# Performance work log

Hardware: AMD Instinct MI355X
Metric: run time of the kernel (lower is better)

Reference implementation:

```python
import jax, jax.numpy as jnp
import numpy as np

L, N, E, H = 2048, 4, 256, 4
D = E // H  # head_dim


def setup_inputs() -> dict:
    key = jax.random.key(0)
    ks = jax.random.split(key, 8)
    s = 1.0 / np.sqrt(E)
    return {
        "x": jax.random.normal(ks[0], (L, N, E), jnp.float32),
        "pos_emb": jax.random.normal(ks[1], (1, 2 * L - 1, E), jnp.float32),
        "in_proj_w": jax.random.normal(ks[2], (3 * E, E), jnp.float32) * s,
        "in_proj_b": jnp.zeros((3 * E,), jnp.float32),
        "pos_w": jax.random.normal(ks[3], (E, E), jnp.float32) * s,
        "pos_bias_u": jax.random.normal(ks[4], (H, D), jnp.float32) * s,
        "pos_bias_v": jax.random.normal(ks[5], (H, D), jnp.float32) * s,
        "out_proj_w": jax.random.normal(ks[6], (E, E), jnp.float32) * s,
        "out_proj_b": jnp.zeros((E,), jnp.float32),
    }


def _rel_shift(bd):
    # bd: (N, H, L, 2L-1) -> (N, H, L, L); out[...,i,j] = bd[...,i, L-1-i+j]
    l = bd.shape[2]
    idx = (l - 1) - jnp.arange(l)[:, None] + jnp.arange(l)[None, :]  # (L, L)
    return jnp.take_along_axis(bd, idx[None, None, :, :], axis=-1)


def reference(x, pos_emb, in_proj_w, in_proj_b, pos_w, pos_bias_u,
              pos_bias_v, out_proj_w, out_proj_b):
    scaling = 1.0 / jnp.sqrt(jnp.asarray(D, x.dtype))
    qkv = x @ in_proj_w.T + in_proj_b                # (L, N, 3E)
    q, k, v = jnp.split(qkv, 3, axis=-1)
    q = q * scaling
    # (L,N,E) -> (N,H,L,D)
    q = q.reshape(L, N, H, D).transpose(1, 2, 0, 3)
    k = k.reshape(L, N, H, D).transpose(1, 2, 0, 3)
    v = v.reshape(L, N, H, D).transpose(1, 2, 0, 3)
    # positional projection: (1, 2L-1, E) -> (H, 2L-1, D)
    p = (pos_emb @ pos_w.T).reshape(2 * L - 1, H, D).transpose(1, 0, 2)
    q_u = q + pos_bias_u[None, :, None, :]
    q_v = q + pos_bias_v[None, :, None, :]
    matrix_ac = jnp.einsum('bhld,bhsd->bhls', q_u, k)          # (N,H,L,L)
    matrix_bd = jnp.einsum('bhld,hnd->bhln', q_v, p)           # (N,H,L,2L-1)
    matrix_bd = _rel_shift(matrix_bd)                          # (N,H,L,L)
    scores = matrix_ac + matrix_bd
    attn = jax.nn.softmax(scores, axis=-1)
    out = jnp.einsum('bhls,bhsd->bhld', attn, v)               # (N,H,L,D)
    out = out.transpose(2, 0, 1, 3).reshape(L, N, E)
    return out @ out_proj_w.T + out_proj_b
```

## Files before the change

### kernel.cpp

```cpp
#include <hip/hip_runtime.h>
#include <math.h>
#include <stdint.h>


typedef __attribute__((ext_vector_type(8))) _Float16 half8;
typedef __attribute__((ext_vector_type(4))) float f32x4;
typedef unsigned short u16;
typedef unsigned int u32;

namespace {
constexpr int L_SEQ  = 2048;
constexpr int NB     = 4;
constexpr int EMB    = 256;
constexpr int NH     = 4;
constexpr int HD     = 64;
constexpr int E3     = 768;
constexpr int M_ROWS = L_SEQ * NB;
constexpr int P_ROWS = 2 * L_SEQ - 1;
}

__device__ __forceinline__ u16 f2h(float x) {
    _Float16 h = (_Float16)x;
    return __builtin_bit_cast(u16, h);
}
__device__ __forceinline__ u32 pk2(float a, float b) {
    return (u32)f2h(a) | ((u32)f2h(b) << 16);
}

template <int MODE>
__global__ __launch_bounds__(256, 2) void proj_gemm(
        const void* __restrict__ Ap, const float* __restrict__ W,
        const float* __restrict__ Wb,
        const float* __restrict__ u_bias, const float* __restrict__ v_bias,
        u16* __restrict__ quB, u16* __restrict__ qvB,
        u16* __restrict__ kB,  u16* __restrict__ vtB,
        u16* __restrict__ o16, float* __restrict__ outf) {
    constexpr int NTILES = (MODE == 0) ? 12 : 4;
    __shared__ __align__(16) u16 ws[64 * 256];

    const int t    = threadIdx.x;
    const int lane = t & 63;
    const int w    = t >> 6;
    const int il   = lane & 15;
    const int g    = lane >> 4;

    const int qq = gridDim.x >> 3;
    const int logical = (blockIdx.x & 7) * qq + (blockIdx.x >> 3);
    const int mt = logical / NTILES, nt = logical % NTILES;
    const int m0 = mt * 64, n0 = nt * 64;

    {
        const int kc = (t & 31) * 8;
        const int rb = t >> 5;
        #pragma unroll
        for (int rr = 0; rr < 8; ++rr) {
            const int row = rb * 8 + rr;
            const float* wr = &W[(size_t)(n0 + row) * 256 + kc];
            float4 f0 = *(const float4*)&wr[0];
            float4 f1 = *(const float4*)&wr[4];
            uint4 pk = make_uint4(pk2(f0.x, f0.y), pk2(f0.z, f0.w),
                                  pk2(f1.x, f1.y), pk2(f1.z, f1.w));
            *(uint4*)((char*)ws + row * 512 + ((kc * 2) ^ ((row & 7) << 4))) = pk;
        }
    }

    const int m = m0 + w * 16 + il;
    half8 bfrag[8];
    if (MODE == 2) {
        const u16* arow = (const u16*)Ap + (size_t)m * 256;
        #pragma unroll
        for (int c = 0; c < 8; ++c)
            bfrag[c] = *(const half8*)&arow[c * 32 + g * 8];
    } else {
        const int mld = (MODE == 1 && m > P_ROWS - 1) ? (P_ROWS - 1) : m;
        const float* arow = (const float*)Ap + (size_t)mld * 256;
        #pragma unroll
        for (int c = 0; c < 8; ++c) {
            float4 f0 = *(const float4*)&arow[c * 32 + g * 8];
            float4 f1 = *(const float4*)&arow[c * 32 + g * 8 + 4];
            uint4 pk = make_uint4(pk2(f0.x, f0.y), pk2(f0.z, f0.w),
                                  pk2(f1.x, f1.y), pk2(f1.z, f1.w));
            bfrag[c] = __builtin_bit_cast(half8, pk);
        }
    }
    __syncthreads();

    f32x4 acc[4] = {};
    __builtin_amdgcn_s_setprio(1);
    #pragma unroll
    for (int c = 0; c < 8; ++c) {
        #pragma unroll
        for (int jt = 0; jt < 4; ++jt) {
            const int row = jt * 16 + il;
            half8 af = *(const half8*)((const char*)ws + row * 512 +
                                       ((c * 64 + g * 16) ^ ((row & 7) << 4)));
            acc[jt] = __builtin_amdgcn_mfma_f32_16x16x32_f16(af, bfrag[c], acc[jt], 0, 0, 0);
        }
    }
    __builtin_amdgcn_s_setprio(0);

    float av[4][4];
    #pragma unroll
    for (int jt = 0; jt < 4; ++jt)
        #pragma unroll
        for (int r = 0; r < 4; ++r)
            av[jt][r] = acc[jt][r] +
                ((MODE != 1) ? Wb[n0 + jt * 16 + g * 4 + r] : 0.f);

    if (MODE == 0) {
        const int seg = nt >> 2;
        const int h   = nt & 3;
        const int i = m >> 2, b = m & 3, bh = b * 4 + h;
        const size_t obase = (((size_t)bh << 11) + i) * 64;
        if (seg == 0) {
            #pragma unroll
            for (int jt = 0; jt < 4; ++jt) {
                const int d0 = jt * 16 + g * 4;
                float uu[4], vv[4];
                #pragma unroll
                for (int r = 0; r < 4; ++r) {
                    uu[r] = av[jt][r] * 0.125f + u_bias[h * 64 + d0 + r];
                    vv[r] = av[jt][r] * 0.125f + v_bias[h * 64 + d0 + r];
                }
                *(uint2*)&quB[obase + d0] = make_uint2(pk2(uu[0], uu[1]), pk2(uu[2], uu[3]));
                *(uint2*)&qvB[obase + d0] = make_uint2(pk2(vv[0], vv[1]), pk2(vv[2], vv[3]));
            }
        } else if (seg == 1) {
            #pragma unroll
            for (int jt = 0; jt < 4; ++jt) {
                const int d0 = jt * 16 + g * 4;
                *(uint2*)&kB[obase + d0] =
                    make_uint2(pk2(av[jt][0], av[jt][1]), pk2(av[jt][2], av[jt][3]));
            }
        } else {
            __syncthreads();
            u16* vt = ws;
            #pragma unroll
            for (int jt = 0; jt < 4; ++jt) {
                *(uint2*)&vt[(w * 16 + il) * 68 + jt * 16 + g * 4] =
                    make_uint2(pk2(av[jt][0], av[jt][1]), pk2(av[jt][2], av[jt][3]));
            }
            __syncthreads();
            const int d = t & 63, bsel = t >> 6;
            u32 pkx[8];
            #pragma unroll
            for (int p2 = 0; p2 < 8; ++p2)
                pkx[p2] = (u32)vt[(p2 * 8 + bsel) * 68 + d] |
                          ((u32)vt[(p2 * 8 + 4 + bsel) * 68 + d] << 16);
            u16* dst = &vtB[(((size_t)(bsel * 4 + h)) * 64 + d) * 2048 + (m0 >> 2)];
            *(uint4*)&dst[0] = make_uint4(pkx[0], pkx[1], pkx[2], pkx[3]);
            *(uint4*)&dst[8] = make_uint4(pkx[4], pkx[5], pkx[6], pkx[7]);
        }
    } else if (MODE == 1) {
        const int h = nt;
        if (m < P_ROWS) {
            #pragma unroll
            for (int jt = 0; jt < 4; ++jt) {
                const int d0 = jt * 16 + g * 4;
                *(uint2*)&o16[((size_t)h * P_ROWS + m) * 64 + d0] =
                    make_uint2(pk2(av[jt][0], av[jt][1]), pk2(av[jt][2], av[jt][3]));
            }
        }
    } else {
        float* orow = &outf[(size_t)m * 256 + n0];
        #pragma unroll
        for (int jt = 0; jt < 4; ++jt) {
            float4 o = make_float4(av[jt][0], av[jt][1], av[jt][2], av[jt][3]);
            *(float4*)&orow[jt * 16 + g * 4] = o;
        }
    }
}

__global__ __launch_bounds__(256, 2) void attn_mfma(
        const u16* __restrict__ quB, const u16* __restrict__ qvB,
        const u16* __restrict__ kB,  const u16* __restrict__ vtB,
        const u16* __restrict__ pB,  u16* __restrict__ attn_out) {
    __shared__ __align__(16) u16   k_s[64 * 64];
    __shared__ __align__(16) u16   v_s[64 * 64];
    __shared__ __align__(16) u16   p_s[128 * 64];
    __shared__ __align__(16) float bd_s[4][16 * 84];
    __shared__ __align__(16) u16   prob_s[4][16 * 64];

    const int t    = threadIdx.x;
    const int lane = t & 63;
    const int w    = t >> 6;
    const int il   = lane & 15;
    const int g    = lane >> 4;

    const int logical = ((blockIdx.x & 7) << 6) + (blockIdx.x >> 3);
    const int bh = logical >> 5;
    const int i0 = (logical & 31) * 64;
    const int b  = bh >> 2, h = bh & 3;

    half8 qu_f[2], qv_f[2];
    {
        const size_t qrow = ((size_t)bh * L_SEQ + i0 + w * 16 + il) * HD;
        qu_f[0] = *(const half8*)&quB[qrow + g * 8];
        qu_f[1] = *(const half8*)&quB[qrow + 32 + g * 8];
        qv_f[0] = *(const half8*)&qvB[qrow + g * 8];
        qv_f[1] = *(const half8*)&qvB[qrow + 32 + g * 8];
    }

    const int r0w = 48 - 16 * w;
    int krd[4][2], prd[5][2], pbrd[2], pwr[4];
    #pragma unroll
    for (int x4 = 0; x4 < 4; ++x4)
        #pragma unroll
        for (int c = 0; c < 2; ++c) {
            int row = x4 * 16 + il;
            krd[x4][c] = row * 128 + ((c * 64 + g * 16) ^ ((row & 7) << 4));
        }
    #pragma unroll
    for (int rt = 0; rt < 5; ++rt)
        #pragma unroll
        for (int c = 0; c < 2; ++c) {
            int row = r0w + rt * 16 + il;
            prd[rt][c] = row * 128 + ((c * 64 + g * 16) ^ ((row & 7) << 4));
        }
    #pragma unroll
    for (int c = 0; c < 2; ++c)
        pbrd[c] = il * 128 + ((c * 64 + g * 16) ^ ((il & 7) << 4));
    #pragma unroll
    for (int jt = 0; jt < 4; ++jt)
        pwr[jt] = il * 128 + (((jt * 16 + g * 4) * 2) ^ ((il & 7) << 4));
    const int bdwr = il * 84 + g * 4;
    const int bdrd = il * 83 + 15 + g * 4;

    f32x4 outacc[4] = {};
    float m_run = -INFINITY, l_run = 0.f;

    for (int kt = 0; kt < 32; ++kt) {
        const int j0 = kt * 64;
        const int nbase = 1984 - i0 + j0;
        __syncthreads();
        {
            const int rw = t >> 3;
            const int a  = t & 7;
            #pragma unroll
            for (int kr = 0; kr < 2; ++kr) {
                const int j = kr * 32 + rw;
                uint4 val = *(const uint4*)&kB[((size_t)bh * L_SEQ + j0 + j) * HD + a * 8];
                *(uint4*)((char*)k_s + (j * 128 + ((a * 16) ^ ((j & 7) << 4)))) = val;
            }
            #pragma unroll
            for (int vr = 0; vr < 2; ++vr) {
                const int d = vr * 32 + rw;
                uint4 val = *(const uint4*)&vtB[((size_t)bh * HD + d) * L_SEQ + j0 + a * 8];
                *(uint4*)((char*)v_s + (d * 128 + ((a * 16) ^ ((d & 7) << 4)))) = val;
            }
            #pragma unroll
            for (int pr = 0; pr < 4; ++pr) {
                const int r = pr * 32 + rw;
                int n = nbase + r; n = n > (P_ROWS - 1) ? (P_ROWS - 1) : n;
                uint4 val = *(const uint4*)&pB[((size_t)h * P_ROWS + n) * HD + a * 8];
                *(uint4*)((char*)p_s + (r * 128 + ((a * 16) ^ ((r & 7) << 4)))) = val;
            }
        }
        __syncthreads();

        __builtin_amdgcn_s_setprio(1);
        #pragma unroll
        for (int rt = 0; rt < 5; ++rt) {
            f32x4 acc = {};
            #pragma unroll
            for (int c = 0; c < 2; ++c) {
                half8 a = *(const half8*)((const char*)p_s + prd[rt][c]);
                acc = __builtin_amdgcn_mfma_f32_16x16x32_f16(a, qv_f[c], acc, 0, 0, 0);
            }
            *(f32x4*)&bd_s[w][bdwr + rt * 16] = acc;
        }
        __builtin_amdgcn_s_setprio(0);

        float sreg[16];
        __builtin_amdgcn_s_setprio(1);
        #pragma unroll
        for (int jt = 0; jt < 4; ++jt) {
            f32x4 acc = {};
            #pragma unroll
            for (int c = 0; c < 2; ++c) {
                half8 a = *(const half8*)((const char*)k_s + krd[jt][c]);
                acc = __builtin_amdgcn_mfma_f32_16x16x32_f16(a, qu_f[c], acc, 0, 0, 0);
            }
            #pragma unroll
            for (int tt = 0; tt < 4; ++tt)
                sreg[jt * 4 + tt] = acc[tt] + bd_s[w][bdrd + jt * 16 + tt];
        }
        __builtin_amdgcn_s_setprio(0);

        float mx = sreg[0];
        #pragma unroll
        for (int z = 1; z < 16; ++z) mx = fmaxf(mx, sreg[z]);
        mx = fmaxf(mx, __shfl_xor(mx, 16));
        mx = fmaxf(mx, __shfl_xor(mx, 32));
        const float m_new = fmaxf(m_run, mx);
        const float corr = __expf(m_run - m_new);
        float lsum = 0.f;
        #pragma unroll
        for (int z = 0; z < 16; ++z) { sreg[z] = __expf(sreg[z] - m_new); lsum += sreg[z]; }
        lsum += __shfl_xor(lsum, 16);
        lsum += __shfl_xor(lsum, 32);
        l_run = l_run * corr + lsum;
        m_run = m_new;
        #pragma unroll
        for (int dt = 0; dt < 4; ++dt) outacc[dt] *= corr;

        #pragma unroll
        for (int jt = 0; jt < 4; ++jt) {
            u32 lo = pk2(sreg[jt * 4 + 0], sreg[jt * 4 + 1]);
            u32 hi = pk2(sreg[jt * 4 + 2], sreg[jt * 4 + 3]);
            *(uint2*)((char*)&prob_s[w][0] + pwr[jt]) = make_uint2(lo, hi);
        }

        half8 pfrag[2];
        #pragma unroll
        for (int c = 0; c < 2; ++c)
            pfrag[c] = *(const half8*)((const char*)&prob_s[w][0] + pbrd[c]);
        __builtin_amdgcn_s_setprio(1);
        #pragma unroll
        for (int dt = 0; dt < 4; ++dt) {
            #pragma unroll
            for (int c = 0; c < 2; ++c) {
                half8 a = *(const half8*)((const char*)v_s + krd[dt][c]);
                outacc[dt] = __builtin_amdgcn_mfma_f32_16x16x32_f16(a, pfrag[c], outacc[dt], 0, 0, 0);
            }
        }
        __builtin_amdgcn_s_setprio(0);
    }

    const float inv = 1.f / l_run;
    const int m = (i0 + w * 16 + il) * NB + b;
    u16* orow = &attn_out[(size_t)m * EMB + h * HD];
    #pragma unroll
    for (int dt = 0; dt < 4; ++dt) {
        u32 lo = pk2(outacc[dt][0] * inv, outacc[dt][1] * inv);
        u32 hi = pk2(outacc[dt][2] * inv, outacc[dt][3] * inv);
        *(uint2*)&orow[dt * 16 + g * 4] = make_uint2(lo, hi);
    }
}

extern "C" void kernel_launch(void* const* d_in, const int* in_sizes, int n_in,
                              void* d_out, int out_size, void* d_ws, size_t ws_size,
                              hipStream_t stream) {
    const float* x        = (const float*)d_in[0];
    const float* pos_emb  = (const float*)d_in[1];
    const float* in_w     = (const float*)d_in[2];
    const float* in_b     = (const float*)d_in[3];
    const float* pos_w    = (const float*)d_in[4];
    const float* u_bias   = (const float*)d_in[5];
    const float* v_bias   = (const float*)d_in[6];
    const float* out_w    = (const float*)d_in[7];
    const float* out_b    = (const float*)d_in[8];
    float* out = (float*)d_out;

    u16* quB   = (u16*)d_ws;
    u16* qvB   = quB + (size_t)16 * L_SEQ * HD;
    u16* kB    = qvB + (size_t)16 * L_SEQ * HD;
    u16* vtB   = kB  + (size_t)16 * L_SEQ * HD;
    u16* pB    = vtB + (size_t)16 * L_SEQ * HD;
    u16* attnb = pB  + (size_t)NH * P_ROWS * HD;

    proj_gemm<0><<<dim3(128 * 12), 256, 0, stream>>>(
        x, in_w, in_b, u_bias, v_bias, quB, qvB, kB, vtB, nullptr, nullptr);
    proj_gemm<1><<<dim3(64 * 4), 256, 0, stream>>>(
        pos_emb, pos_w, nullptr, nullptr, nullptr,
        nullptr, nullptr, nullptr, nullptr, pB, nullptr);
    attn_mfma<<<dim3(512), 256, 0, stream>>>(quB, qvB, kB, vtB, pB, attnb);
    proj_gemm<2><<<dim3(128 * 4), 256, 0, stream>>>(
        attnb, out_w, out_b, nullptr, nullptr,
        nullptr, nullptr, nullptr, nullptr, nullptr, out);
}
```

Measured before the change: 169.9 us.

## Reuse weight tiles across M subtiles, stage coalesced stores, prefetch attention tiles

The projection GEMM now processes several 64-row M subtiles per block (MSUB), so each block loads and converts the weight tile once. The next A subtile is prefetched into registers while the current one computes. Q/K/V outputs are staged through a shared scratch buffer so global writes become full 16-byte coalesced rows. The V transpose now covers a full 64-position span. The attention kernel prefetches the next K/V/P tile into registers during the current tile's compute. This trades fewer blocks and more register and LDS use, which may lower occupancy, for reduced redundant weight loading and better overlap of global loads.

```diff
diff --git a/kernel.cpp b/kernel.cpp
--- a/kernel.cpp
+++ b/kernel.cpp
@@ -27,7 +27,7 @@
     return (u32)f2h(a) | ((u32)f2h(b) << 16);
 }
 
-template <int MODE>
+template <int MODE, int MSUB>
 __global__ __launch_bounds__(256, 2) void proj_gemm(
         const void* __restrict__ Ap, const float* __restrict__ W,
         const float* __restrict__ Wb,
@@ -35,8 +35,10 @@
         u16* __restrict__ quB, u16* __restrict__ qvB,
         u16* __restrict__ kB,  u16* __restrict__ vtB,
         u16* __restrict__ o16, float* __restrict__ outf) {
-    constexpr int NTILES = (MODE == 0) ? 12 : 4;
+    constexpr int NT   = (MODE == 0) ? 12 : 4;
+    constexpr int SCRN = (MODE == 0) ? (4 * 64 * 72) : (MODE == 1 ? 64 * 72 : 8);
     __shared__ __align__(16) u16 ws[64 * 256];
+    __shared__ __align__(16) u16 scr[SCRN];
 
     const int t    = threadIdx.x;
     const int lane = t & 63;
@@ -46,15 +48,49 @@
 
     const int qq = gridDim.x >> 3;
     const int logical = (blockIdx.x & 7) * qq + (blockIdx.x >> 3);
-    const int mt = logical / NTILES, nt = logical % NTILES;
-    const int m0 = mt * 64, n0 = nt * 64;
-
+    const int mg = logical / NT, nt = logical % NT;
+    const int n0 = nt * 64;
+
+    half8 bf[2][8];
+    float4 ra[2][8], rb[2][8];
+
+    auto issueA = [&](int s, int p) {
+        const int m_ = (mg * MSUB + s) * 64 + w * 16 + il;
+        if constexpr (MODE == 2) {
+            const u16* ar = (const u16*)Ap + (size_t)m_ * 256;
+            #pragma unroll
+            for (int c = 0; c < 8; ++c)
+                bf[p][c] = *(const half8*)&ar[c * 32 + g * 8];
+        } else {
+            const int mld = (MODE == 1 && m_ > P_ROWS - 1) ? (P_ROWS - 1) : m_;
+            const float* ar = (const float*)Ap + (size_t)mld * 256;
+            #pragma unroll
+            for (int c = 0; c < 8; ++c) {
+                ra[p][c] = *(const float4*)&ar[c * 32 + g * 8];
+                rb[p][c] = *(const float4*)&ar[c * 32 + g * 8 + 4];
+            }
+        }
+    };
+    auto packA = [&](int p) {
+        if constexpr (MODE != 2) {
+            #pragma unroll
+            for (int c = 0; c < 8; ++c) {
+                uint4 pk = make_uint4(pk2(ra[p][c].x, ra[p][c].y),
+                                      pk2(ra[p][c].z, ra[p][c].w),
+                                      pk2(rb[p][c].x, rb[p][c].y),
+                                      pk2(rb[p][c].z, rb[p][c].w));
+                bf[p][c] = __builtin_bit_cast(half8, pk);
+            }
+        }
+    };
+
+    issueA(0, 0);
     {
         const int kc = (t & 31) * 8;
-        const int rb = t >> 5;
+        const int rb_ = t >> 5;
         #pragma unroll
         for (int rr = 0; rr < 8; ++rr) {
-            const int row = rb * 8 + rr;
+            const int row = rb_ * 8 + rr;
             const float* wr = &W[(size_t)(n0 + row) * 256 + kc];
             float4 f0 = *(const float4*)&wr[0];
             float4 f1 = *(const float4*)&wr[4];
@@ -63,110 +99,152 @@
             *(uint4*)((char*)ws + row * 512 + ((kc * 2) ^ ((row & 7) << 4))) = pk;
         }
     }
-
-    const int m = m0 + w * 16 + il;
-    half8 bfrag[8];
-    if (MODE == 2) {
-        const u16* arow = (const u16*)Ap + (size_t)m * 256;
-        #pragma unroll
-        for (int c = 0; c < 8; ++c)
-            bfrag[c] = *(const half8*)&arow[c * 32 + g * 8];
-    } else {
-        const int mld = (MODE == 1 && m > P_ROWS - 1) ? (P_ROWS - 1) : m;
-        const float* arow = (const float*)Ap + (size_t)mld * 256;
+    packA(0);
+    __syncthreads();
+
+    const int seg = (MODE == 0) ? (nt >> 2) : 0;
+    const int h   = (MODE == 0) ? (nt & 3) : nt;
+
+    #pragma unroll
+    for (int s = 0; s < MSUB; ++s) {
+        if (s + 1 < MSUB) issueA(s + 1, (s + 1) & 1);
+
+        f32x4 acc[4] = {};
         #pragma unroll
         for (int c = 0; c < 8; ++c) {
-            float4 f0 = *(const float4*)&arow[c * 32 + g * 8];
-            float4 f1 = *(const float4*)&arow[c * 32 + g * 8 + 4];
-            uint4 pk = make_uint4(pk2(f0.x, f0.y), pk2(f0.z, f0.w),
-                                  pk2(f1.x, f1.y), pk2(f1.z, f1.w));
-            bfrag[c] = __builtin_bit_cast(half8, pk);
-        }
-    }
-    __syncthreads();
-
-    f32x4 acc[4] = {};
-    __builtin_amdgcn_s_setprio(1);
-    #pragma unroll
-    for (int c = 0; c < 8; ++c) {
-        #pragma unroll
-        for (int jt = 0; jt < 4; ++jt) {
-            const int row = jt * 16 + il;
-            half8 af = *(const half8*)((const char*)ws + row * 512 +
-                                       ((c * 64 + g * 16) ^ ((row & 7) << 4)));
-            acc[jt] = __builtin_amdgcn_mfma_f32_16x16x32_f16(af, bfrag[c], acc[jt], 0, 0, 0);
-        }
-    }
-    __builtin_amdgcn_s_setprio(0);
-
-    float av[4][4];
-    #pragma unroll
-    for (int jt = 0; jt < 4; ++jt)
-        #pragma unroll
-        for (int r = 0; r < 4; ++r)
-            av[jt][r] = acc[jt][r] +
-                ((MODE != 1) ? Wb[n0 + jt * 16 + g * 4 + r] : 0.f);
-
-    if (MODE == 0) {
-        const int seg = nt >> 2;
-        const int h   = nt & 3;
-        const int i = m >> 2, b = m & 3, bh = b * 4 + h;
-        const size_t obase = (((size_t)bh << 11) + i) * 64;
-        if (seg == 0) {
+            #pragma unroll
+            for (int jt = 0; jt < 4; ++jt) {
+                const int row = jt * 16 + il;
+                half8 af = *(const half8*)((const char*)ws + row * 512 +
+                                           ((c * 64 + g * 16) ^ ((row & 7) << 4)));
+                acc[jt] = __builtin_amdgcn_mfma_f32_16x16x32_f16(af, bf[s & 1][c], acc[jt], 0, 0, 0);
+            }
+        }
+
+        float av[4][4];
+        #pragma unroll
+        for (int jt = 0; jt < 4; ++jt)
+            #pragma unroll
+            for (int r = 0; r < 4; ++r)
+                av[jt][r] = acc[jt][r] +
+                    ((MODE != 1) ? Wb[n0 + jt * 16 + g * 4 + r] : 0.f);
+
+        const int s64  = (mg * MSUB + s) * 64;
+        const int mloc = w * 16 + il;
+
+        if constexpr (MODE == 0) {
+            if (seg == 0) {
+                const int i0g = s64 >> 2;
+                __syncthreads();
+                #pragma unroll
+                for (int jt = 0; jt < 4; ++jt) {
+                    const int d0 = jt * 16 + g * 4;
+                    float uu[4];
+                    #pragma unroll
+                    for (int r = 0; r < 4; ++r)
+                        uu[r] = av[jt][r] * 0.125f + u_bias[h * 64 + d0 + r];
+                    *(uint2*)&scr[mloc * 72 + d0] = make_uint2(pk2(uu[0], uu[1]), pk2(uu[2], uu[3]));
+                }
+                __syncthreads();
+                {
+                    const int b_ = t >> 6, iL = (t >> 2) & 15, dq = (t & 3) * 16;
+                    uint4 v0 = *(const uint4*)&scr[(iL * 4 + b_) * 72 + dq];
+                    uint4 v1 = *(const uint4*)&scr[(iL * 4 + b_) * 72 + dq + 8];
+                    u16* dst = &quB[(((size_t)(b_ * 4 + h)) * 2048 + i0g + iL) * 64 + dq];
+                    *(uint4*)&dst[0] = v0; *(uint4*)&dst[8] = v1;
+                }
+                __syncthreads();
+                #pragma unroll
+                for (int jt = 0; jt < 4; ++jt) {
+                    const int d0 = jt * 16 + g * 4;
+                    float vv[4];
+                    #pragma unroll
+                    for (int r = 0; r < 4; ++r)
+                        vv[r] = av[jt][r] * 0.125f + v_bias[h * 64 + d0 + r];
+                    *(uint2*)&scr[mloc * 72 + d0] = make_uint2(pk2(vv[0], vv[1]), pk2(vv[2], vv[3]));
+                }
+                __syncthreads();
+                {
+                    const int b_ = t >> 6, iL = (t >> 2) & 15, dq = (t & 3) * 16;
+                    uint4 v0 = *(const uint4*)&scr[(iL * 4 + b_) * 72 + dq];
+                    uint4 v1 = *(const uint4*)&scr[(iL * 4 + b_) * 72 + dq + 8];
+                    u16* dst = &qvB[(((size_t)(b_ * 4 + h)) * 2048 + i0g + iL) * 64 + dq];
+                    *(uint4*)&dst[0] = v0; *(uint4*)&dst[8] = v1;
+                }
+            } else if (seg == 1) {
+                const int i0g = s64 >> 2;
+                __syncthreads();
+                #pragma unroll
+                for (int jt = 0; jt < 4; ++jt) {
+                    const int d0 = jt * 16 + g * 4;
+                    *(uint2*)&scr[mloc * 72 + d0] =
+                        make_uint2(pk2(av[jt][0], av[jt][1]), pk2(av[jt][2], av[jt][3]));
+                }
+                __syncthreads();
+                {
+                    const int b_ = t >> 6, iL = (t >> 2) & 15, dq = (t & 3) * 16;
+                    uint4 v0 = *(const uint4*)&scr[(iL * 4 + b_) * 72 + dq];
+                    uint4 v1 = *(const uint4*)&scr[(iL * 4 + b_) * 72 + dq + 8];
+                    u16* dst = &kB[(((size_t)(b_ * 4 + h)) * 2048 + i0g + iL) * 64 + dq];
+                    *(uint4*)&dst[0] = v0; *(uint4*)&dst[8] = v1;
+                }
+            } else {
+                const int b_ = il & 3;
+                const int jl = s * 16 + w * 4 + (il >> 2);
+                #pragma unroll
+                for (int jt = 0; jt < 4; ++jt) {
+                    const int d0 = jt * 16 + g * 4;
+                    *(uint2*)&scr[(b_ * 64 + jl) * 72 + d0] =
+                        make_uint2(pk2(av[jt][0], av[jt][1]), pk2(av[jt][2], av[jt][3]));
+                }
+            }
+        } else if constexpr (MODE == 1) {
+            __syncthreads();
             #pragma unroll
             for (int jt = 0; jt < 4; ++jt) {
                 const int d0 = jt * 16 + g * 4;
-                float uu[4], vv[4];
+                *(uint2*)&scr[mloc * 72 + d0] =
+                    make_uint2(pk2(av[jt][0], av[jt][1]), pk2(av[jt][2], av[jt][3]));
+            }
+            __syncthreads();
+            {
+                const int nL = t >> 2, dq = (t & 3) * 16;
+                const int mrow = s64 + nL;
+                if (mrow < P_ROWS) {
+                    uint4 v0 = *(const uint4*)&scr[nL * 72 + dq];
+                    uint4 v1 = *(const uint4*)&scr[nL * 72 + dq + 8];
+                    u16* dst = &o16[((size_t)h * P_ROWS + mrow) * 64 + dq];
+                    *(uint4*)&dst[0] = v0; *(uint4*)&dst[8] = v1;
+                }
+            }
+        } else {
+            const int m_ = s64 + mloc;
+            float* orow = &outf[(size_t)m_ * 256 + n0];
+            #pragma unroll
+            for (int jt = 0; jt < 4; ++jt)
+                *(float4*)&orow[jt * 16 + g * 4] =
+                    make_float4(av[jt][0], av[jt][1], av[jt][2], av[jt][3]);
+        }
+
+        if (s + 1 < MSUB) packA((s + 1) & 1);
+    }
+
+    if constexpr (MODE == 0) {
+        if (seg == 2) {
+            __syncthreads();
+            const int jbase = mg * 64;
+            #pragma unroll
+            for (int b_ = 0; b_ < 4; ++b_) {
+                const int d = t >> 2, jc = (t & 3) * 16;
+                u32 pkx[8];
                 #pragma unroll
-                for (int r = 0; r < 4; ++r) {
-                    uu[r] = av[jt][r] * 0.125f + u_bias[h * 64 + d0 + r];
-                    vv[r] = av[jt][r] * 0.125f + v_bias[h * 64 + d0 + r];
-                }
-                *(uint2*)&quB[obase + d0] = make_uint2(pk2(uu[0], uu[1]), pk2(uu[2], uu[3]));
-                *(uint2*)&qvB[obase + d0] = make_uint2(pk2(vv[0], vv[1]), pk2(vv[2], vv[3]));
-            }
-        } else if (seg == 1) {
-            #pragma unroll
-            for (int jt = 0; jt < 4; ++jt) {
-                const int d0 = jt * 16 + g * 4;
-                *(uint2*)&kB[obase + d0] =
-                    make_uint2(pk2(av[jt][0], av[jt][1]), pk2(av[jt][2], av[jt][3]));
-            }
-        } else {
-            __syncthreads();
-            u16* vt = ws;
-            #pragma unroll
-            for (int jt = 0; jt < 4; ++jt) {
-                *(uint2*)&vt[(w * 16 + il) * 68 + jt * 16 + g * 4] =
-                    make_uint2(pk2(av[jt][0], av[jt][1]), pk2(av[jt][2], av[jt][3]));
-            }
-            __syncthreads();
-            const int d = t & 63, bsel = t >> 6;
-            u32 pkx[8];
-            #pragma unroll
-            for (int p2 = 0; p2 < 8; ++p2)
-                pkx[p2] = (u32)vt[(p2 * 8 + bsel) * 68 + d] |
-                          ((u32)vt[(p2 * 8 + 4 + bsel) * 68 + d] << 16);
-            u16* dst = &vtB[(((size_t)(bsel * 4 + h)) * 64 + d) * 2048 + (m0 >> 2)];
-            *(uint4*)&dst[0] = make_uint4(pkx[0], pkx[1], pkx[2], pkx[3]);
-            *(uint4*)&dst[8] = make_uint4(pkx[4], pkx[5], pkx[6], pkx[7]);
-        }
-    } else if (MODE == 1) {
-        const int h = nt;
-        if (m < P_ROWS) {
-            #pragma unroll
-            for (int jt = 0; jt < 4; ++jt) {
-                const int d0 = jt * 16 + g * 4;
-                *(uint2*)&o16[((size_t)h * P_ROWS + m) * 64 + d0] =
-                    make_uint2(pk2(av[jt][0], av[jt][1]), pk2(av[jt][2], av[jt][3]));
-            }
-        }
-    } else {
-        float* orow = &outf[(size_t)m * 256 + n0];
-        #pragma unroll
-        for (int jt = 0; jt < 4; ++jt) {
-            float4 o = make_float4(av[jt][0], av[jt][1], av[jt][2], av[jt][3]);
-            *(float4*)&orow[jt * 16 + g * 4] = o;
+                for (int z = 0; z < 8; ++z)
+                    pkx[z] = (u32)scr[(b_ * 64 + jc + 2 * z) * 72 + d] |
+                             ((u32)scr[(b_ * 64 + jc + 2 * z + 1) * 72 + d] << 16);
+                u16* dst = &vtB[(((size_t)(b_ * 4 + h)) * 64 + d) * 2048 + jbase + jc];
+                *(uint4*)&dst[0] = make_uint4(pkx[0], pkx[1], pkx[2], pkx[3]);
+                *(uint4*)&dst[8] = make_uint4(pkx[4], pkx[5], pkx[6], pkx[7]);
+            }
         }
     }
 }
@@ -226,36 +304,55 @@
     const int bdwr = il * 84 + g * 4;
     const int bdrd = il * 83 + 15 + g * 4;
 
+    const int rw = t >> 3, a8 = t & 7;
+    int kds[2], vds[2], pds[4];
+    #pragma unroll
+    for (int kr = 0; kr < 2; ++kr) {
+        const int j = kr * 32 + rw;
+        kds[kr] = j * 128 + ((a8 * 16) ^ ((j & 7) << 4));
+    }
+    #pragma unroll
+    for (int vr = 0; vr < 2; ++vr) {
+        const int d = vr * 32 + rw;
+        vds[vr] = d * 128 + ((a8 * 16) ^ ((d & 7) << 4));
+    }
+    #pragma unroll
+    for (int pr = 0; pr < 4; ++pr) {
+        const int r = pr * 32 + rw;
+        pds[pr] = r * 128 + ((a8 * 16) ^ ((r & 7) << 4));
+    }
+    uint4 kreg[2], vreg[2], preg[4];
+    auto stageLoad = [&](int kt) {
+        #pragma unroll
+        for (int kr = 0; kr < 2; ++kr)
+            kreg[kr] = *(const uint4*)&kB[((size_t)bh * 2048 + kt * 64 + kr * 32 + rw) * 64 + a8 * 8];
+        #pragma unroll
+        for (int vr = 0; vr < 2; ++vr)
+            vreg[vr] = *(const uint4*)&vtB[((size_t)bh * 64 + vr * 32 + rw) * 2048 + (size_t)kt * 64 + a8 * 8];
+        #pragma unroll
+        for (int pr = 0; pr < 4; ++pr) {
+            int n = 1984 - i0 + kt * 64 + pr * 32 + rw;
+            n = n > (P_ROWS - 1) ? (P_ROWS - 1) : n;
+            preg[pr] = *(const uint4*)&pB[((size_t)h * P_ROWS + n) * 64 + a8 * 8];
+        }
+    };
+
     f32x4 outacc[4] = {};
     float m_run = -INFINITY, l_run = 0.f;
 
+    stageLoad(0);
     for (int kt = 0; kt < 32; ++kt) {
-        const int j0 = kt * 64;
-        const int nbase = 1984 - i0 + j0;
         __syncthreads();
-        {
-            const int rw = t >> 3;
-            const int a  = t & 7;
-            #pragma unroll
-            for (int kr = 0; kr < 2; ++kr) {
-                const int j = kr * 32 + rw;
-                uint4 val = *(const uint4*)&kB[((size_t)bh * L_SEQ + j0 + j) * HD + a * 8];
-                *(uint4*)((char*)k_s + (j * 128 + ((a * 16) ^ ((j & 7) << 4)))) = val;
-            }
-            #pragma unroll
-            for (int vr = 0; vr < 2; ++vr) {
-                const int d = vr * 32 + rw;
-                uint4 val = *(const uint4*)&vtB[((size_t)bh * HD + d) * L_SEQ + j0 + a * 8];
-                *(uint4*)((char*)v_s + (d * 128 + ((a * 16) ^ ((d & 7) << 4)))) = val;
-            }
-            #pragma unroll
-            for (int pr = 0; pr < 4; ++pr) {
-                const int r = pr * 32 + rw;
-                int n = nbase + r; n = n > (P_ROWS - 1) ? (P_ROWS - 1) : n;
-                uint4 val = *(const uint4*)&pB[((size_t)h * P_ROWS + n) * HD + a * 8];
-                *(uint4*)((char*)p_s + (r * 128 + ((a * 16) ^ ((r & 7) << 4)))) = val;
-            }
-        }
+        #pragma unroll
+        for (int kr = 0; kr < 2; ++kr)
+            *(uint4*)((char*)k_s + kds[kr]) = kreg[kr];
+        #pragma unroll
+        for (int vr = 0; vr < 2; ++vr)
+            *(uint4*)((char*)v_s + vds[vr]) = vreg[vr];
+        #pragma unroll
+        for (int pr = 0; pr < 4; ++pr)
+            *(uint4*)((char*)p_s + pds[pr]) = preg[pr];
+        if (kt < 31) stageLoad(kt + 1);
         __syncthreads();
 
         __builtin_amdgcn_s_setprio(1);
@@ -359,13 +456,13 @@
     u16* pB    = vtB + (size_t)16 * L_SEQ * HD;
     u16* attnb = pB  + (size_t)NH * P_ROWS * HD;
 
-    proj_gemm<0><<<dim3(128 * 12), 256, 0, stream>>>(
+    proj_gemm<0, 4><<<dim3(32 * 12), 256, 0, stream>>>(
         x, in_w, in_b, u_bias, v_bias, quB, qvB, kB, vtB, nullptr, nullptr);
-    proj_gemm<1><<<dim3(64 * 4), 256, 0, stream>>>(
+    proj_gemm<1, 1><<<dim3(64 * 4), 256, 0, stream>>>(
         pos_emb, pos_w, nullptr, nullptr, nullptr,
         nullptr, nullptr, nullptr, nullptr, pB, nullptr);
     attn_mfma<<<dim3(512), 256, 0, stream>>>(quB, qvB, kB, vtB, pB, attnb);
-    proj_gemm<2><<<dim3(128 * 4), 256, 0, stream>>>(
+    proj_gemm<2, 2><<<dim3(64 * 4), 256, 0, stream>>>(
         attnb, out_w, out_b, nullptr, nullptr,
         nullptr, nullptr, nullptr, nullptr, nullptr, out);
 }
```

Result: slower. 233.3 us (+37.3%).

## Merge QKV and positional projections into one launch with 128-row tiles

Applied to the files above, without the earlier changes.

Combines the QKV projection and the positional projection into a single kernel launch, dispatching on the logical block index. Each block now covers 128 rows instead of 64, so the converted weight tile in shared memory is reused across twice as many rows. Q/K/P outputs are staged through a per-wave shared scratch buffer so global stores are full 16-byte row writes, and the output GEMM gets the same 128-row tiling. This cuts one launch and redundant weight conversion, at the cost of more registers, more shared memory per block and fewer blocks in flight.

```diff
diff --git a/kernel.cpp b/kernel.cpp
--- a/kernel.cpp
+++ b/kernel.cpp
@@ -14,8 +14,6 @@
 constexpr int EMB    = 256;
 constexpr int NH     = 4;
 constexpr int HD     = 64;
-constexpr int E3     = 768;
-constexpr int M_ROWS = L_SEQ * NB;
 constexpr int P_ROWS = 2 * L_SEQ - 1;
 }
 
@@ -27,16 +25,15 @@
     return (u32)f2h(a) | ((u32)f2h(b) << 16);
 }
 
-template <int MODE>
-__global__ __launch_bounds__(256, 2) void proj_gemm(
-        const void* __restrict__ Ap, const float* __restrict__ W,
-        const float* __restrict__ Wb,
+__global__ __launch_bounds__(256, 2) void qkvpos_gemm(
+        const float* __restrict__ x, const float* __restrict__ pos_emb,
+        const float* __restrict__ in_w, const float* __restrict__ in_b,
+        const float* __restrict__ pos_w,
         const float* __restrict__ u_bias, const float* __restrict__ v_bias,
         u16* __restrict__ quB, u16* __restrict__ qvB,
-        u16* __restrict__ kB,  u16* __restrict__ vtB,
-        u16* __restrict__ o16, float* __restrict__ outf) {
-    constexpr int NTILES = (MODE == 0) ? 12 : 4;
+        u16* __restrict__ kB,  u16* __restrict__ vtB, u16* __restrict__ pB) {
     __shared__ __align__(16) u16 ws[64 * 256];
+    __shared__ __align__(16) u16 scr[128 * 72];
 
     const int t    = threadIdx.x;
     const int lane = t & 63;
@@ -44,48 +41,53 @@
     const int il   = lane & 15;
     const int g    = lane >> 4;
 
-    const int qq = gridDim.x >> 3;
-    const int logical = (blockIdx.x & 7) * qq + (blockIdx.x >> 3);
-    const int mt = logical / NTILES, nt = logical % NTILES;
-    const int m0 = mt * 64, n0 = nt * 64;
+    const int logical = (blockIdx.x & 7) * 112 + (blockIdx.x >> 3);
+    const bool isQKV = logical < 768;
+    int mg, nt;
+    const float *Ap, *W, *Wb;
+    if (isQKV) { mg = logical / 12; nt = logical % 12; Ap = x;       W = in_w;  Wb = in_b; }
+    else       { const int l2 = logical - 768;
+                 mg = l2 >> 2;     nt = l2 & 3;      Ap = pos_emb; W = pos_w; Wb = nullptr; }
+    const int m0 = mg * 128, n0 = nt * 64;
 
     {
-        const int kc = (t & 31) * 8;
-        const int rb = t >> 5;
+        const int kc = (t & 31) * 8, rb_ = t >> 5;
         #pragma unroll
         for (int rr = 0; rr < 8; ++rr) {
-            const int row = rb * 8 + rr;
+            const int row = rb_ * 8 + rr;
             const float* wr = &W[(size_t)(n0 + row) * 256 + kc];
             float4 f0 = *(const float4*)&wr[0];
             float4 f1 = *(const float4*)&wr[4];
-            uint4 pk = make_uint4(pk2(f0.x, f0.y), pk2(f0.z, f0.w),
-                                  pk2(f1.x, f1.y), pk2(f1.z, f1.w));
-            *(uint4*)((char*)ws + row * 512 + ((kc * 2) ^ ((row & 7) << 4))) = pk;
-        }
-    }
-
-    const int m = m0 + w * 16 + il;
-    half8 bfrag[8];
-    if (MODE == 2) {
-        const u16* arow = (const u16*)Ap + (size_t)m * 256;
-        #pragma unroll
-        for (int c = 0; c < 8; ++c)
-            bfrag[c] = *(const half8*)&arow[c * 32 + g * 8];
-    } else {
-        const int mld = (MODE == 1 && m > P_ROWS - 1) ? (P_ROWS - 1) : m;
-        const float* arow = (const float*)Ap + (size_t)mld * 256;
+            *(uint4*)((char*)ws + row * 512 + ((kc * 2) ^ ((row & 7) << 4))) =
+                make_uint4(pk2(f0.x, f0.y), pk2(f0.z, f0.w),
+                           pk2(f1.x, f1.y), pk2(f1.z, f1.w));
+        }
+    }
+
+    half8 bf0[8], bf1[8];
+    {
+        int r0 = m0 + w * 32 + il;
+        int r1 = r0 + 16;
+        if (!isQKV) { r0 = r0 > 4094 ? 4094 : r0; r1 = r1 > 4094 ? 4094 : r1; }
+        const float* a0 = Ap + (size_t)r0 * 256;
+        const float* a1 = Ap + (size_t)r1 * 256;
         #pragma unroll
         for (int c = 0; c < 8; ++c) {
-            float4 f0 = *(const float4*)&arow[c * 32 + g * 8];
-            float4 f1 = *(const float4*)&arow[c * 32 + g * 8 + 4];
-            uint4 pk = make_uint4(pk2(f0.x, f0.y), pk2(f0.z, f0.w),
-                                  pk2(f1.x, f1.y), pk2(f1.z, f1.w));
-            bfrag[c] = __builtin_bit_cast(half8, pk);
+            float4 f0 = *(const float4*)&a0[c * 32 + g * 8];
+            float4 f1 = *(const float4*)&a0[c * 32 + g * 8 + 4];
+            bf0[c] = __builtin_bit_cast(half8,
+                make_uint4(pk2(f0.x, f0.y), pk2(f0.z, f0.w),
+                           pk2(f1.x, f1.y), pk2(f1.z, f1.w)));
+            float4 h0 = *(const float4*)&a1[c * 32 + g * 8];
+            float4 h1 = *(const float4*)&a1[c * 32 + g * 8 + 4];
+            bf1[c] = __builtin_bit_cast(half8,
+                make_uint4(pk2(h0.x, h0.y), pk2(h0.z, h0.w),
+                           pk2(h1.x, h1.y), pk2(h1.z, h1.w)));
         }
     }
     __syncthreads();
 
-    f32x4 acc[4] = {};
+    f32x4 acc0[4] = {}, acc1[4] = {};
     __builtin_amdgcn_s_setprio(1);
     #pragma unroll
     for (int c = 0; c < 8; ++c) {
@@ -94,79 +96,158 @@
             const int row = jt * 16 + il;
             half8 af = *(const half8*)((const char*)ws + row * 512 +
                                        ((c * 64 + g * 16) ^ ((row & 7) << 4)));
-            acc[jt] = __builtin_amdgcn_mfma_f32_16x16x32_f16(af, bfrag[c], acc[jt], 0, 0, 0);
+            acc0[jt] = __builtin_amdgcn_mfma_f32_16x16x32_f16(af, bf0[c], acc0[jt], 0, 0, 0);
+            acc1[jt] = __builtin_amdgcn_mfma_f32_16x16x32_f16(af, bf1[c], acc1[jt], 0, 0, 0);
         }
     }
     __builtin_amdgcn_s_setprio(0);
 
-    float av[4][4];
+    float av[2][4][4];
     #pragma unroll
     for (int jt = 0; jt < 4; ++jt)
         #pragma unroll
-        for (int r = 0; r < 4; ++r)
-            av[jt][r] = acc[jt][r] +
-                ((MODE != 1) ? Wb[n0 + jt * 16 + g * 4 + r] : 0.f);
-
-    if (MODE == 0) {
-        const int seg = nt >> 2;
-        const int h   = nt & 3;
-        const int i = m >> 2, b = m & 3, bh = b * 4 + h;
-        const size_t obase = (((size_t)bh << 11) + i) * 64;
-        if (seg == 0) {
+        for (int r = 0; r < 4; ++r) {
+            const float bb = Wb ? Wb[n0 + jt * 16 + g * 4 + r] : 0.f;
+            av[0][jt][r] = acc0[jt][r] + bb;
+            av[1][jt][r] = acc1[jt][r] + bb;
+        }
+
+    u16* scrw = scr + w * (32 * 72);
+    const int rrd  = lane >> 1;
+    const int base = (lane & 1) * 32;
+
+    auto waveStore = [&](u16* dstBase, int hh, float scale, const float* bias,
+                         bool qkvLayout) {
+        #pragma unroll
+        for (int s = 0; s < 2; ++s)
             #pragma unroll
             for (int jt = 0; jt < 4; ++jt) {
                 const int d0 = jt * 16 + g * 4;
-                float uu[4], vv[4];
+                float v0 = av[s][jt][0] * scale, v1 = av[s][jt][1] * scale;
+                float v2 = av[s][jt][2] * scale, v3 = av[s][jt][3] * scale;
+                if (bias) {
+                    v0 += bias[hh * 64 + d0 + 0]; v1 += bias[hh * 64 + d0 + 1];
+                    v2 += bias[hh * 64 + d0 + 2]; v3 += bias[hh * 64 + d0 + 3];
+                }
+                *(uint2*)&scrw[(s * 16 + il) * 72 + d0] = make_uint2(pk2(v0, v1), pk2(v2, v3));
+            }
+        uint4 q0 = *(const uint4*)&scrw[rrd * 72 + base + 0];
+        uint4 q1 = *(const uint4*)&scrw[rrd * 72 + base + 8];
+        uint4 q2 = *(const uint4*)&scrw[rrd * 72 + base + 16];
+        uint4 q3 = *(const uint4*)&scrw[rrd * 72 + base + 24];
+        const int mglob = m0 + w * 32 + rrd;
+        if (qkvLayout) {
+            const int i = mglob >> 2, b = mglob & 3;
+            u16* dp = dstBase + (((size_t)(b * 4 + hh)) * 2048 + i) * 64 + base;
+            *(uint4*)&dp[0] = q0; *(uint4*)&dp[8] = q1;
+            *(uint4*)&dp[16] = q2; *(uint4*)&dp[24] = q3;
+        } else if (mglob < P_ROWS) {
+            u16* dp = dstBase + ((size_t)hh * P_ROWS + mglob) * 64 + base;
+            *(uint4*)&dp[0] = q0; *(uint4*)&dp[8] = q1;
+            *(uint4*)&dp[16] = q2; *(uint4*)&dp[24] = q3;
+        }
+    };
+
+    if (isQKV) {
+        const int seg = nt >> 2, h = nt & 3;
+        if (seg == 0) {
+            waveStore(quB, h, 0.125f, u_bias, true);
+            waveStore(qvB, h, 0.125f, v_bias, true);
+        } else if (seg == 1) {
+            waveStore(kB, h, 1.f, nullptr, true);
+        } else {
+            #pragma unroll
+            for (int s = 0; s < 2; ++s)
                 #pragma unroll
-                for (int r = 0; r < 4; ++r) {
-                    uu[r] = av[jt][r] * 0.125f + u_bias[h * 64 + d0 + r];
-                    vv[r] = av[jt][r] * 0.125f + v_bias[h * 64 + d0 + r];
-                }
-                *(uint2*)&quB[obase + d0] = make_uint2(pk2(uu[0], uu[1]), pk2(uu[2], uu[3]));
-                *(uint2*)&qvB[obase + d0] = make_uint2(pk2(vv[0], vv[1]), pk2(vv[2], vv[3]));
-            }
-        } else if (seg == 1) {
-            #pragma unroll
-            for (int jt = 0; jt < 4; ++jt) {
-                const int d0 = jt * 16 + g * 4;
-                *(uint2*)&kB[obase + d0] =
-                    make_uint2(pk2(av[jt][0], av[jt][1]), pk2(av[jt][2], av[jt][3]));
-            }
-        } else {
+                for (int jt = 0; jt < 4; ++jt)
+                    *(uint2*)&scr[(w * 32 + s * 16 + il) * 72 + jt * 16 + g * 4] =
+                        make_uint2(pk2(av[s][jt][0], av[s][jt][1]),
+                                   pk2(av[s][jt][2], av[s][jt][3]));
             __syncthreads();
-            u16* vt = ws;
-            #pragma unroll
-            for (int jt = 0; jt < 4; ++jt) {
-                *(uint2*)&vt[(w * 16 + il) * 68 + jt * 16 + g * 4] =
-                    make_uint2(pk2(av[jt][0], av[jt][1]), pk2(av[jt][2], av[jt][3]));
-            }
-            __syncthreads();
-            const int d = t & 63, bsel = t >> 6;
-            u32 pkx[8];
-            #pragma unroll
-            for (int p2 = 0; p2 < 8; ++p2)
-                pkx[p2] = (u32)vt[(p2 * 8 + bsel) * 68 + d] |
-                          ((u32)vt[(p2 * 8 + 4 + bsel) * 68 + d] << 16);
-            u16* dst = &vtB[(((size_t)(bsel * 4 + h)) * 64 + d) * 2048 + (m0 >> 2)];
-            *(uint4*)&dst[0] = make_uint4(pkx[0], pkx[1], pkx[2], pkx[3]);
-            *(uint4*)&dst[8] = make_uint4(pkx[4], pkx[5], pkx[6], pkx[7]);
-        }
-    } else if (MODE == 1) {
-        const int h = nt;
-        if (m < P_ROWS) {
-            #pragma unroll
-            for (int jt = 0; jt < 4; ++jt) {
-                const int d0 = jt * 16 + g * 4;
-                *(uint2*)&o16[((size_t)h * P_ROWS + m) * 64 + d0] =
-                    make_uint2(pk2(av[jt][0], av[jt][1]), pk2(av[jt][2], av[jt][3]));
-            }
+            const int b_ = w, d = lane;
+            u32 pkx[16];
+            #pragma unroll
+            for (int z = 0; z < 16; ++z)
+                pkx[z] = (u32)scr[((2 * z) * 4 + b_) * 72 + d] |
+                         ((u32)scr[((2 * z + 1) * 4 + b_) * 72 + d] << 16);
+            u16* dp = vtB + (((size_t)(b_ * 4 + h)) * 64 + d) * 2048 + mg * 32;
+            *(uint4*)&dp[0]  = make_uint4(pkx[0],  pkx[1],  pkx[2],  pkx[3]);
+            *(uint4*)&dp[8]  = make_uint4(pkx[4],  pkx[5],  pkx[6],  pkx[7]);
+            *(uint4*)&dp[16] = make_uint4(pkx[8],  pkx[9],  pkx[10], pkx[11]);
+            *(uint4*)&dp[24] = make_uint4(pkx[12], pkx[13], pkx[14], pkx[15]);
         }
     } else {
-        float* orow = &outf[(size_t)m * 256 + n0];
+        waveStore(pB, nt, 1.f, nullptr, false);
+    }
+}
+
+__global__ __launch_bounds__(256, 2) void out_gemm(
+        const u16* __restrict__ attnb, const float* __restrict__ W,
+        const float* __restrict__ Wb, float* __restrict__ outf) {
+    __shared__ __align__(16) u16 ws[64 * 256];
+
+    const int t    = threadIdx.x;
+    const int lane = t & 63;
+    const int w    = t >> 6;
+    const int il   = lane & 15;
+    const int g    = lane >> 4;
+
+    const int logical = (blockIdx.x & 7) * 32 + (blockIdx.x >> 3);
+    const int mg = logical >> 2, nt = logical & 3;
+    const int m0 = mg * 128, n0 = nt * 64;
+
+    {
+        const int kc = (t & 31) * 8, rb_ = t >> 5;
+        #pragma unroll
+        for (int rr = 0; rr < 8; ++rr) {
+            const int row = rb_ * 8 + rr;
+            const float* wr = &W[(size_t)(n0 + row) * 256 + kc];
+            float4 f0 = *(const float4*)&wr[0];
+            float4 f1 = *(const float4*)&wr[4];
+            *(uint4*)((char*)ws + row * 512 + ((kc * 2) ^ ((row & 7) << 4))) =
+                make_uint4(pk2(f0.x, f0.y), pk2(f0.z, f0.w),
+                           pk2(f1.x, f1.y), pk2(f1.z, f1.w));
+        }
+    }
+    half8 bf0[8], bf1[8];
+    {
+        const u16* a0 = attnb + (size_t)(m0 + w * 32 + il) * 256;
+        const u16* a1 = a0 + 16 * 256;
+        #pragma unroll
+        for (int c = 0; c < 8; ++c) {
+            bf0[c] = *(const half8*)&a0[c * 32 + g * 8];
+            bf1[c] = *(const half8*)&a1[c * 32 + g * 8];
+        }
+    }
+    __syncthreads();
+
+    f32x4 acc0[4] = {}, acc1[4] = {};
+    __builtin_amdgcn_s_setprio(1);
+    #pragma unroll
+    for (int c = 0; c < 8; ++c) {
         #pragma unroll
         for (int jt = 0; jt < 4; ++jt) {
-            float4 o = make_float4(av[jt][0], av[jt][1], av[jt][2], av[jt][3]);
-            *(float4*)&orow[jt * 16 + g * 4] = o;
+            const int row = jt * 16 + il;
+            half8 af = *(const half8*)((const char*)ws + row * 512 +
+                                       ((c * 64 + g * 16) ^ ((row & 7) << 4)));
+            acc0[jt] = __builtin_amdgcn_mfma_f32_16x16x32_f16(af, bf0[c], acc0[jt], 0, 0, 0);
+            acc1[jt] = __builtin_amdgcn_mfma_f32_16x16x32_f16(af, bf1[c], acc1[jt], 0, 0, 0);
+        }
+    }
+    __builtin_amdgcn_s_setprio(0);
+
+    #pragma unroll
+    for (int s = 0; s < 2; ++s) {
+        const int m_ = m0 + w * 32 + s * 16 + il;
+        float* orow = &outf[(size_t)m_ * 256 + n0];
+        #pragma unroll
+        for (int jt = 0; jt < 4; ++jt) {
+            const f32x4 a = s ? acc1[jt] : acc0[jt];
+            *(float4*)&orow[jt * 16 + g * 4] = make_float4(
+                a[0] + Wb[n0 + jt * 16 + g * 4 + 0],
+                a[1] + Wb[n0 + jt * 16 + g * 4 + 1],
+                a[2] + Wb[n0 + jt * 16 + g * 4 + 2],
+                a[3] + Wb[n0 + jt * 16 + g * 4 + 3]);
         }
     }
 }
@@ -359,13 +440,8 @@
     u16* pB    = vtB + (size_t)16 * L_SEQ * HD;
     u16* attnb = pB  + (size_t)NH * P_ROWS * HD;
 
-    proj_gemm<0><<<dim3(128 * 12), 256, 0, stream>>>(
-        x, in_w, in_b, u_bias, v_bias, quB, qvB, kB, vtB, nullptr, nullptr);
-    proj_gemm<1><<<dim3(64 * 4), 256, 0, stream>>>(
-        pos_emb, pos_w, nullptr, nullptr, nullptr,
-        nullptr, nullptr, nullptr, nullptr, pB, nullptr);
+    qkvpos_gemm<<<dim3(896), 256, 0, stream>>>(
+        x, pos_emb, in_w, in_b, pos_w, u_bias, v_bias, quB, qvB, kB, vtB, pB);
     attn_mfma<<<dim3(512), 256, 0, stream>>>(quB, qvB, kB, vtB, pB, attnb);
-    proj_gemm<2><<<dim3(128 * 4), 256, 0, stream>>>(
-        attnb, out_w, out_b, nullptr, nullptr,
-        nullptr, nullptr, nullptr, nullptr, nullptr, out);
-}
+    out_gemm<<<dim3(256), 256, 0, stream>>>(attnb, out_w, out_b, out);
+}
```

After: 171.4 us. Within noise of the previous version (+0.9%).
